# Performance work log

Hardware: AMD Instinct MI355X
Metric: run time of the kernel (lower is better)

Reference implementation:

```python
import jax, jax.numpy as jnp
import numpy as np

N_HEADS = 16
D_MODEL = 1024
D_K = D_MODEL // N_HEADS
B, S = 2, 2048


def setup_inputs() -> dict:
    key = jax.random.key(0)
    ks = jax.random.split(key, 12)
    sc = 1.0 / np.sqrt(D_MODEL)
    inp = {
        'query': jax.random.normal(ks[0], (B, S, D_MODEL), jnp.float32),
        'key':   jax.random.normal(ks[1], (B, S, D_MODEL), jnp.float32),
        'value': jax.random.normal(ks[2], (B, S, D_MODEL), jnp.float32),
        'mask':  jnp.ones((B, 1, 1, S), jnp.int32),
        'Wq': jax.random.normal(ks[3], (D_MODEL, D_MODEL), jnp.float32) * sc,
        'bq': jnp.zeros((D_MODEL,), jnp.float32),
        'Wk': jax.random.normal(ks[4], (D_MODEL, D_MODEL), jnp.float32) * sc,
        'bk': jnp.zeros((D_MODEL,), jnp.float32),
        'Wv': jax.random.normal(ks[5], (D_MODEL, D_MODEL), jnp.float32) * sc,
        'bv': jnp.zeros((D_MODEL,), jnp.float32),
        'Wo': jax.random.normal(ks[6], (D_MODEL, D_MODEL), jnp.float32) * sc,
        'bo': jnp.zeros((D_MODEL,), jnp.float32),
    }
    return inp


def reference(query, key, value, mask, Wq, bq, Wk, bk, Wv, bv, Wo, bo):
    # Linear projections (torch Linear: x @ W.T + b)
    q = query @ Wq.T + bq
    k = key @ Wk.T + bk
    v = value @ Wv.T + bv
    # [B, S, D] -> [B, H, S, d_k]
    def split_heads(x):
        b, s, _ = x.shape
        return x.reshape(b, s, N_HEADS, D_K).transpose(0, 2, 1, 3)
    q, k, v = split_heads(q), split_heads(k), split_heads(v)
    # scaled dot-product attention with explicit [B,H,S,S] scores
    att = jnp.einsum('bhqd,bhkd->bhqk', q, k) / jnp.sqrt(jnp.float32(D_K))
    att = jnp.where(mask == 0, -jnp.inf, att)
    scores = jax.nn.softmax(att, axis=-1)
    # dropout is identity in eval/reference mode
    out = jnp.einsum('bhqk,bhkd->bhqd', scores, v)
    b = out.shape[0]
    out = out.transpose(0, 2, 1, 3).reshape(b, -1, N_HEADS * D_K)
    return out @ Wo.T + bo
```

## Files before the change

kernel.cpp:

```cpp
#include <hip/hip_runtime.h>
#include <hip/hip_bf16.h>

#define DM   1024
#define SLEN 2048
#define NH   16
#define DK   64

typedef float f32x4 __attribute__((ext_vector_type(4)));
typedef short short8 __attribute__((ext_vector_type(8)));

__device__ __forceinline__ unsigned short f2bf(float f) {
  union { float f; unsigned int u; } x; x.f = f;
  unsigned int r = x.u + 0x7fffu + ((x.u >> 16) & 1u);
  return (unsigned short)(r >> 16);
}

__device__ __forceinline__ void gload_lds16(const unsigned short* g, unsigned short* l) {
  __builtin_amdgcn_global_load_lds(
      (const __attribute__((address_space(1))) unsigned int*)g,
      (__attribute__((address_space(3))) unsigned int*)l, 16, 0, 0);
}

struct ConvArgs { const float* src[7]; unsigned short* dst[7]; };

__global__ __launch_bounds__(256) void conv_kernel(ConvArgs a) {
  int blk = blockIdx.x, seg, base;
  if (blk < 6144) { seg = blk >> 11; base = blk & 2047; }
  else { int t = blk - 6144; seg = 3 + (t >> 9); base = t & 511; }
  const float* s = a.src[seg];
  unsigned short* d = a.dst[seg];
  int idx = (base * 256 + (int)threadIdx.x) * 8;
  float4 v0 = *(const float4*)(s + idx);
  float4 v1 = *(const float4*)(s + idx + 4);
  unsigned short o[8];
  o[0]=f2bf(v0.x); o[1]=f2bf(v0.y); o[2]=f2bf(v0.z); o[3]=f2bf(v0.w);
  o[4]=f2bf(v1.x); o[5]=f2bf(v1.y); o[6]=f2bf(v1.z); o[7]=f2bf(v1.w);
  *(uint4*)(d + idx) = *(uint4*)o;
}

template <int MODE>
__device__ __forceinline__ void gemm_core(const unsigned short* __restrict__ A,
                                          const unsigned short* __restrict__ W,
                                          const float* __restrict__ bias,
                                          void* __restrict__ outp, float scale,
                                          int m0, int n0,
                                          unsigned short* As, unsigned short* Bs) {
  const int tid = threadIdx.x;
  const int lane = tid & 63;
  const int wv = tid >> 6;
  const int wm = (wv >> 1) * 64, wn = (wv & 1) * 64;

  f32x4 acc[4][4];
#pragma unroll
  for (int i = 0; i < 4; ++i)
#pragma unroll
    for (int j = 0; j < 4; ++j) acc[i][j] = (f32x4){0.f, 0.f, 0.f, 0.f};

  for (int k0 = 0; k0 < DM; k0 += 32) {
    __syncthreads();
#pragma unroll
    for (int i = 0; i < 2; ++i) {
      int c = tid + i * 256;
      int row = c >> 2, cs = (c & 3) << 3;
      gload_lds16(A + (size_t)(m0 + row) * DM + k0 + cs, As + c * 8);
      gload_lds16(W + (size_t)(n0 + row) * DM + k0 + cs, Bs + c * 8);
    }
    __syncthreads();
    short8 af[4], bf[4];
#pragma unroll
    for (int i = 0; i < 4; ++i)
      af[i] = *(const short8*)(As + (wm + i * 16 + (lane & 15)) * 32 + ((lane >> 4) << 3));
#pragma unroll
    for (int j = 0; j < 4; ++j)
      bf[j] = *(const short8*)(Bs + (wn + j * 16 + (lane & 15)) * 32 + ((lane >> 4) << 3));
#pragma unroll
    for (int i = 0; i < 4; ++i)
#pragma unroll
      for (int j = 0; j < 4; ++j)
        acc[i][j] = __builtin_amdgcn_mfma_f32_16x16x32_bf16(af[i], bf[j], acc[i][j], 0, 0, 0);
  }

#pragma unroll
  for (int i = 0; i < 4; ++i)
#pragma unroll
    for (int j = 0; j < 4; ++j) {
      int col = n0 + wn + j * 16 + (lane & 15);
      float bv = bias[col];
      int row0 = m0 + wm + i * 16 + ((lane >> 4) << 2);
      if (MODE == 2) {
        unsigned short pk[4];
#pragma unroll
        for (int g = 0; g < 4; ++g) pk[g] = f2bf(acc[i][j][g] + bv);
        int d = col & (DK - 1), hh = col >> 6;
        int brow = row0 >> 11, srow = row0 & (SLEN - 1);
        size_t idx = ((size_t)((brow * NH + hh) * DK + d)) * SLEN + srow;
        *(uint2*)(((unsigned short*)outp) + idx) = *(uint2*)pk;
      } else {
#pragma unroll
        for (int g = 0; g < 4; ++g) {
          int row = row0 + g;
          float v = acc[i][j][g] + bv;
          if (MODE == 0) {
            v *= scale;
            size_t idx = ((size_t)((row >> 11) * NH + (col >> 6))) * (SLEN * DK) +
                         (size_t)(row & (SLEN - 1)) * DK + (col & (DK - 1));
            ((unsigned short*)outp)[idx] = f2bf(v);
          } else {
            ((float*)outp)[(size_t)row * DM + col] = v;
          }
        }
      }
    }
}

struct QKArgs {
  const unsigned short* A[2];
  const unsigned short* W[2];
  const float* bias[2];
  unsigned short* out[2];
  float scale[2];
};

__global__ __launch_bounds__(256) void gemm_qk_kernel(QKArgs a) {
  __shared__ unsigned short As[128 * 32], Bs[128 * 32];
  int z = blockIdx.z;
  gemm_core<0>(a.A[z], a.W[z], a.bias[z], a.out[z], a.scale[z],
               blockIdx.x * 128, blockIdx.y * 128, As, Bs);
}

__global__ __launch_bounds__(256) void gemm_v_kernel(const unsigned short* __restrict__ A,
                                                     const unsigned short* __restrict__ W,
                                                     const float* __restrict__ bias,
                                                     unsigned short* __restrict__ out) {
  __shared__ unsigned short As[128 * 32], Bs[128 * 32];
  gemm_core<2>(A, W, bias, out, 1.0f, blockIdx.x * 128, blockIdx.y * 128, As, Bs);
}

__global__ __launch_bounds__(256) void gemm_o_kernel(const unsigned short* __restrict__ A,
                                                     const unsigned short* __restrict__ W,
                                                     const float* __restrict__ bias,
                                                     float* __restrict__ out) {
  __shared__ unsigned short As[128 * 32], Bs[128 * 32];
  gemm_core<1>(A, W, bias, out, 1.0f, blockIdx.x * 128, blockIdx.y * 128, As, Bs);
}

__global__ __launch_bounds__(256) void attn_kernel(
    const unsigned short* __restrict__ Qw,
    const unsigned short* __restrict__ Kw,
    const unsigned short* __restrict__ Vtw,
    const int* __restrict__ mask,
    unsigned short* __restrict__ attn_out) {
  __shared__ unsigned short QPs[128 * 72];
  __shared__ unsigned short Ks[64 * 72];
  __shared__ unsigned short Vts[64 * 72];
  __shared__ float maskadd[64];

  const int tid = threadIdx.x;
  const int lane = tid & 63;
  const int wv = tid >> 6;
  const int s0 = blockIdx.x * 128;
  const int bh = blockIdx.y;
  const int b = bh >> 4, h = bh & 15;
  const unsigned short* Qb = Qw + (size_t)bh * (SLEN * DK);
  const unsigned short* Kb = Kw + (size_t)bh * (SLEN * DK);
  const unsigned short* Vtb = Vtw + (size_t)bh * (SLEN * DK);

#pragma unroll
  for (int i = 0; i < 4; ++i) {
    int seg = tid + i * 256;
    int row = seg >> 3, d0 = (seg & 7) << 3;
    *(uint4*)(QPs + row * 72 + d0) = *(const uint4*)(Qb + (size_t)(s0 + row) * DK + d0);
  }

  const int srow = tid >> 3, scol = (tid & 7) << 3;
  const int srow2 = (tid + 256) >> 3, scol2 = ((tid + 256) & 7) << 3;
  uint4 kreg[2], vreg[2];
  int mreg = 1;
  {
    kreg[0] = *(const uint4*)(Kb + (size_t)srow * DK + scol);
    kreg[1] = *(const uint4*)(Kb + (size_t)srow2 * DK + scol2);
    vreg[0] = *(const uint4*)(Vtb + (size_t)srow * SLEN + scol);
    vreg[1] = *(const uint4*)(Vtb + (size_t)srow2 * SLEN + scol2);
    if (tid < 64) mreg = mask[b * SLEN + tid];
  }

  __syncthreads();
  const int qb = wv * 32;
  short8 aq[2][2];
#pragma unroll
  for (int r = 0; r < 2; ++r)
#pragma unroll
    for (int ks = 0; ks < 2; ++ks)
      aq[r][ks] = *(const short8*)(QPs + (qb + r * 16 + (lane & 15)) * 72 + ks * 32 + ((lane >> 4) << 3));

  float lsum[2][4];
  f32x4 O[2][4];
#pragma unroll
  for (int r = 0; r < 2; ++r)
#pragma unroll
    for (int g = 0; g < 4; ++g) {
      lsum[r][g] = 0.f;
      O[r][g] = (f32x4){0.f, 0.f, 0.f, 0.f};
    }

  for (int kt = 0; kt < SLEN / 64; ++kt) {
    if (kt) __syncthreads();
    *(uint4*)(Ks + srow * 72 + scol) = kreg[0];
    *(uint4*)(Ks + srow2 * 72 + scol2) = kreg[1];
    *(uint4*)(Vts + srow * 72 + scol) = vreg[0];
    *(uint4*)(Vts + srow2 * 72 + scol2) = vreg[1];
    if (tid < 64) maskadd[tid] = mreg ? 0.0f : -1e30f;
    __syncthreads();
    if (kt < SLEN / 64 - 1) {
      const int kv1 = (kt + 1) * 64;
      kreg[0] = *(const uint4*)(Kb + (size_t)(kv1 + srow) * DK + scol);
      kreg[1] = *(const uint4*)(Kb + (size_t)(kv1 + srow2) * DK + scol2);
      vreg[0] = *(const uint4*)(Vtb + (size_t)srow * SLEN + kv1 + scol);
      vreg[1] = *(const uint4*)(Vtb + (size_t)srow2 * SLEN + kv1 + scol2);
      if (tid < 64) mreg = mask[b * SLEN + kv1 + tid];
    }

    f32x4 sc[2][4];
#pragma unroll
    for (int c = 0; c < 4; ++c) {
      short8 bk0 = *(const short8*)(Ks + (c * 16 + (lane & 15)) * 72 + ((lane >> 4) << 3));
      short8 bk1 = *(const short8*)(Ks + (c * 16 + (lane & 15)) * 72 + 32 + ((lane >> 4) << 3));
#pragma unroll
      for (int r = 0; r < 2; ++r) {
        f32x4 z = (f32x4){0.f, 0.f, 0.f, 0.f};
        z = __builtin_amdgcn_mfma_f32_16x16x32_bf16(aq[r][0], bk0, z, 0, 0, 0);
        sc[r][c] = __builtin_amdgcn_mfma_f32_16x16x32_bf16(aq[r][1], bk1, z, 0, 0, 0);
      }
    }

    __hip_bfloat16* Pp = (__hip_bfloat16*)QPs;
#pragma unroll
    for (int c = 0; c < 4; ++c) {
      float ma = maskadd[c * 16 + (lane & 15)];
      int colp = c * 16 + (lane & 15);
#pragma unroll
      for (int r = 0; r < 2; ++r) {
        float p0 = __builtin_exp2f(sc[r][c][0] + ma);
        float p1 = __builtin_exp2f(sc[r][c][1] + ma);
        float p2 = __builtin_exp2f(sc[r][c][2] + ma);
        float p3 = __builtin_exp2f(sc[r][c][3] + ma);
        lsum[r][0] += p0; lsum[r][1] += p1; lsum[r][2] += p2; lsum[r][3] += p3;
        __hip_bfloat162 h01 = __float22bfloat162_rn(float2{p0, p1});
        __hip_bfloat162 h23 = __float22bfloat162_rn(float2{p2, p3});
        int row0 = qb + r * 16 + ((lane >> 4) << 2);
        Pp[(row0 + 0) * 72 + colp] = h01.x;
        Pp[(row0 + 1) * 72 + colp] = h01.y;
        Pp[(row0 + 2) * 72 + colp] = h23.x;
        Pp[(row0 + 3) * 72 + colp] = h23.y;
      }
    }

    short8 ap[2][2];
#pragma unroll
    for (int r = 0; r < 2; ++r)
#pragma unroll
      for (int ks = 0; ks < 2; ++ks)
        ap[r][ks] = *(const short8*)(QPs + (qb + r * 16 + (lane & 15)) * 72 + ks * 32 + ((lane >> 4) << 3));
#pragma unroll
    for (int dt = 0; dt < 4; ++dt) {
      short8 bv0 = *(const short8*)(Vts + (dt * 16 + (lane & 15)) * 72 + ((lane >> 4) << 3));
      short8 bv1 = *(const short8*)(Vts + (dt * 16 + (lane & 15)) * 72 + 32 + ((lane >> 4) << 3));
#pragma unroll
      for (int r = 0; r < 2; ++r) {
        O[r][dt] = __builtin_amdgcn_mfma_f32_16x16x32_bf16(ap[r][0], bv0, O[r][dt], 0, 0, 0);
        O[r][dt] = __builtin_amdgcn_mfma_f32_16x16x32_bf16(ap[r][1], bv1, O[r][dt], 0, 0, 0);
      }
    }
  }

#pragma unroll
  for (int r = 0; r < 2; ++r)
#pragma unroll
    for (int g = 0; g < 4; ++g) {
      float rs = lsum[r][g];
      rs += __shfl_xor(rs, 1);
      rs += __shfl_xor(rs, 2);
      rs += __shfl_xor(rs, 4);
      rs += __shfl_xor(rs, 8);
      float inv = 1.0f / rs;
      int row = s0 + qb + r * 16 + ((lane >> 4) << 2) + g;
#pragma unroll
      for (int dt = 0; dt < 4; ++dt) {
        int col = h * DK + dt * 16 + (lane & 15);
        attn_out[(size_t)(b * SLEN + row) * DM + col] = f2bf(O[r][dt][g] * inv);
      }
    }
}

extern "C" void kernel_launch(void* const* d_in, const int* in_sizes, int n_in,
                              void* d_out, int out_size, void* d_ws, size_t ws_size,
                              hipStream_t stream) {
  (void)in_sizes; (void)n_in; (void)out_size; (void)ws_size;
  const float* query = (const float*)d_in[0];
  const float* key_  = (const float*)d_in[1];
  const float* value = (const float*)d_in[2];
  const int*   mask  = (const int*)d_in[3];
  const float* Wq = (const float*)d_in[4];
  const float* bq = (const float*)d_in[5];
  const float* Wk = (const float*)d_in[6];
  const float* bk = (const float*)d_in[7];
  const float* Wv = (const float*)d_in[8];
  const float* bv = (const float*)d_in[9];
  const float* Wo = (const float*)d_in[10];
  const float* bo = (const float*)d_in[11];
  float* out = (float*)d_out;

  const size_t WSZ = 1048576, XSZ = 4194304;
  unsigned short* base = (unsigned short*)d_ws;
  unsigned short* Wqb = base;
  unsigned short* Wkb = base + WSZ;
  unsigned short* Wvb = base + 2 * WSZ;
  unsigned short* Wob = base + 3 * WSZ;
  unsigned short* Xqb = base + 4 * WSZ;
  unsigned short* Xkb = Xqb + XSZ;
  unsigned short* Xvb = Xqb + 2 * XSZ;
  unsigned short* Qw  = Xqb + 3 * XSZ;
  unsigned short* Kw  = Qw + XSZ;
  unsigned short* Vtw = Qw + 2 * XSZ;
  unsigned short* attnb = Qw + 3 * XSZ;

  ConvArgs ca;
  ca.src[0] = query; ca.src[1] = key_; ca.src[2] = value;
  ca.src[3] = Wq; ca.src[4] = Wk; ca.src[5] = Wv; ca.src[6] = Wo;
  ca.dst[0] = Xqb; ca.dst[1] = Xkb; ca.dst[2] = Xvb;
  ca.dst[3] = Wqb; ca.dst[4] = Wkb; ca.dst[5] = Wvb; ca.dst[6] = Wob;
  conv_kernel<<<8192, 256, 0, stream>>>(ca);

  QKArgs qa;
  qa.A[0] = Xqb; qa.A[1] = Xkb;
  qa.W[0] = Wqb; qa.W[1] = Wkb;
  qa.bias[0] = bq; qa.bias[1] = bk;
  qa.out[0] = Qw; qa.out[1] = Kw;
  qa.scale[0] = 0.18033688011112042f;
  qa.scale[1] = 1.0f;
  gemm_qk_kernel<<<dim3(32, 8, 2), 256, 0, stream>>>(qa);
  gemm_v_kernel<<<dim3(32, 8), 256, 0, stream>>>(Xvb, Wvb, bv, Vtw);

  attn_kernel<<<dim3(16, 32), 256, 0, stream>>>(Qw, Kw, Vtw, mask, attnb);

  gemm_o_kernel<<<dim3(32, 8), 256, 0, stream>>>(attnb, Wob, bo, out);
}
```

Baseline: 295.6 us.

## Merge QKV GEMM launches, halve O-GEMM tile N, use 8 waves in attention

The V projection now runs in the same launch as Q and K, selected by a runtime mode per z-slice, which removes one launch and lets the three projections share the GPU. The output projection uses 128x64 tiles, doubling its block count for better CU fill. The attention kernel runs 512 threads with each wave owning 16 query rows instead of 32. This halves per-wave register state and raises the wave count, but each K/V tile is now reused by fewer MFMAs per wave.

```diff
diff --git a/kernel.cpp b/kernel.cpp
--- a/kernel.cpp
+++ b/kernel.cpp
@@ -38,8 +38,9 @@
   *(uint4*)(d + idx) = *(uint4*)o;
 }
 
-template <int MODE>
-__device__ __forceinline__ void gemm_core(const unsigned short* __restrict__ A,
+template <int TN>
+__device__ __forceinline__ void gemm_core(int mode,
+                                          const unsigned short* __restrict__ A,
                                           const unsigned short* __restrict__ W,
                                           const float* __restrict__ bias,
                                           void* __restrict__ outp, float scale,
@@ -48,46 +49,50 @@
   const int tid = threadIdx.x;
   const int lane = tid & 63;
   const int wv = tid >> 6;
-  const int wm = (wv >> 1) * 64, wn = (wv & 1) * 64;
-
-  f32x4 acc[4][4];
+  const int wm = (wv >> 1) * 64, wn = (wv & 1) * (TN / 2);
+  const int NB = TN / 32;
+
+  f32x4 acc[4][NB];
 #pragma unroll
   for (int i = 0; i < 4; ++i)
 #pragma unroll
-    for (int j = 0; j < 4; ++j) acc[i][j] = (f32x4){0.f, 0.f, 0.f, 0.f};
+    for (int j = 0; j < NB; ++j) acc[i][j] = (f32x4){0.f, 0.f, 0.f, 0.f};
 
   for (int k0 = 0; k0 < DM; k0 += 32) {
     __syncthreads();
 #pragma unroll
     for (int i = 0; i < 2; ++i) {
       int c = tid + i * 256;
-      int row = c >> 2, cs = (c & 3) << 3;
-      gload_lds16(A + (size_t)(m0 + row) * DM + k0 + cs, As + c * 8);
-      gload_lds16(W + (size_t)(n0 + row) * DM + k0 + cs, Bs + c * 8);
+      gload_lds16(A + (size_t)(m0 + (c >> 2)) * DM + k0 + ((c & 3) << 3), As + c * 8);
+    }
+#pragma unroll
+    for (int i = 0; i < TN / 64; ++i) {
+      int c = tid + i * 256;
+      gload_lds16(W + (size_t)(n0 + (c >> 2)) * DM + k0 + ((c & 3) << 3), Bs + c * 8);
     }
     __syncthreads();
-    short8 af[4], bf[4];
+    short8 af[4], bf[NB];
 #pragma unroll
     for (int i = 0; i < 4; ++i)
       af[i] = *(const short8*)(As + (wm + i * 16 + (lane & 15)) * 32 + ((lane >> 4) << 3));
 #pragma unroll
-    for (int j = 0; j < 4; ++j)
+    for (int j = 0; j < NB; ++j)
       bf[j] = *(const short8*)(Bs + (wn + j * 16 + (lane & 15)) * 32 + ((lane >> 4) << 3));
 #pragma unroll
     for (int i = 0; i < 4; ++i)
 #pragma unroll
-      for (int j = 0; j < 4; ++j)
+      for (int j = 0; j < NB; ++j)
         acc[i][j] = __builtin_amdgcn_mfma_f32_16x16x32_bf16(af[i], bf[j], acc[i][j], 0, 0, 0);
   }
 
 #pragma unroll
   for (int i = 0; i < 4; ++i)
 #pragma unroll
-    for (int j = 0; j < 4; ++j) {
+    for (int j = 0; j < NB; ++j) {
       int col = n0 + wn + j * 16 + (lane & 15);
       float bv = bias[col];
-      int row0 = m0 + wm + i * 16 + ((lane >> 4) << 2);
-      if (MODE == 2) {
+      int row0 = wm + i * 16 + ((lane >> 4) << 2) + m0;
+      if (mode == 2) {
         unsigned short pk[4];
 #pragma unroll
         for (int g = 0; g < 4; ++g) pk[g] = f2bf(acc[i][j][g] + bv);
@@ -95,56 +100,48 @@
         int brow = row0 >> 11, srow = row0 & (SLEN - 1);
         size_t idx = ((size_t)((brow * NH + hh) * DK + d)) * SLEN + srow;
         *(uint2*)(((unsigned short*)outp) + idx) = *(uint2*)pk;
-      } else {
+      } else if (mode == 0) {
 #pragma unroll
         for (int g = 0; g < 4; ++g) {
           int row = row0 + g;
-          float v = acc[i][j][g] + bv;
-          if (MODE == 0) {
-            v *= scale;
-            size_t idx = ((size_t)((row >> 11) * NH + (col >> 6))) * (SLEN * DK) +
-                         (size_t)(row & (SLEN - 1)) * DK + (col & (DK - 1));
-            ((unsigned short*)outp)[idx] = f2bf(v);
-          } else {
-            ((float*)outp)[(size_t)row * DM + col] = v;
-          }
+          float v = (acc[i][j][g] + bv) * scale;
+          size_t idx = ((size_t)((row >> 11) * NH + (col >> 6))) * (SLEN * DK) +
+                       (size_t)(row & (SLEN - 1)) * DK + (col & (DK - 1));
+          ((unsigned short*)outp)[idx] = f2bf(v);
         }
+      } else {
+#pragma unroll
+        for (int g = 0; g < 4; ++g)
+          ((float*)outp)[(size_t)(row0 + g) * DM + col] = acc[i][j][g] + bv;
       }
     }
 }
 
-struct QKArgs {
-  const unsigned short* A[2];
-  const unsigned short* W[2];
-  const float* bias[2];
-  unsigned short* out[2];
-  float scale[2];
+struct QKVArgs {
+  const unsigned short* A[3];
+  const unsigned short* W[3];
+  const float* bias[3];
+  unsigned short* out[3];
+  float scale[3];
+  int mode[3];
 };
 
-__global__ __launch_bounds__(256) void gemm_qk_kernel(QKArgs a) {
+__global__ __launch_bounds__(256) void gemm_qkv_kernel(QKVArgs a) {
   __shared__ unsigned short As[128 * 32], Bs[128 * 32];
   int z = blockIdx.z;
-  gemm_core<0>(a.A[z], a.W[z], a.bias[z], a.out[z], a.scale[z],
-               blockIdx.x * 128, blockIdx.y * 128, As, Bs);
-}
-
-__global__ __launch_bounds__(256) void gemm_v_kernel(const unsigned short* __restrict__ A,
-                                                     const unsigned short* __restrict__ W,
-                                                     const float* __restrict__ bias,
-                                                     unsigned short* __restrict__ out) {
-  __shared__ unsigned short As[128 * 32], Bs[128 * 32];
-  gemm_core<2>(A, W, bias, out, 1.0f, blockIdx.x * 128, blockIdx.y * 128, As, Bs);
+  gemm_core<128>(a.mode[z], a.A[z], a.W[z], a.bias[z], a.out[z], a.scale[z],
+                 blockIdx.x * 128, blockIdx.y * 128, As, Bs);
 }
 
 __global__ __launch_bounds__(256) void gemm_o_kernel(const unsigned short* __restrict__ A,
                                                      const unsigned short* __restrict__ W,
                                                      const float* __restrict__ bias,
                                                      float* __restrict__ out) {
-  __shared__ unsigned short As[128 * 32], Bs[128 * 32];
-  gemm_core<1>(A, W, bias, out, 1.0f, blockIdx.x * 128, blockIdx.y * 128, As, Bs);
-}
-
-__global__ __launch_bounds__(256) void attn_kernel(
+  __shared__ unsigned short As[128 * 32], Bs[64 * 32];
+  gemm_core<64>(1, A, W, bias, out, 1.0f, blockIdx.x * 128, blockIdx.y * 64, As, Bs);
+}
+
+__global__ __launch_bounds__(512) void attn_kernel(
     const unsigned short* __restrict__ Qw,
     const unsigned short* __restrict__ Kw,
     const unsigned short* __restrict__ Vtw,
@@ -166,130 +163,99 @@
   const unsigned short* Vtb = Vtw + (size_t)bh * (SLEN * DK);
 
 #pragma unroll
-  for (int i = 0; i < 4; ++i) {
-    int seg = tid + i * 256;
+  for (int i = 0; i < 2; ++i) {
+    int seg = tid + i * 512;
     int row = seg >> 3, d0 = (seg & 7) << 3;
     *(uint4*)(QPs + row * 72 + d0) = *(const uint4*)(Qb + (size_t)(s0 + row) * DK + d0);
   }
 
   const int srow = tid >> 3, scol = (tid & 7) << 3;
-  const int srow2 = (tid + 256) >> 3, scol2 = ((tid + 256) & 7) << 3;
-  uint4 kreg[2], vreg[2];
-  int mreg = 1;
-  {
-    kreg[0] = *(const uint4*)(Kb + (size_t)srow * DK + scol);
-    kreg[1] = *(const uint4*)(Kb + (size_t)srow2 * DK + scol2);
-    vreg[0] = *(const uint4*)(Vtb + (size_t)srow * SLEN + scol);
-    vreg[1] = *(const uint4*)(Vtb + (size_t)srow2 * SLEN + scol2);
-    if (tid < 64) mreg = mask[b * SLEN + tid];
-  }
+  uint4 kreg = *(const uint4*)(Kb + (size_t)srow * DK + scol);
+  uint4 vreg = *(const uint4*)(Vtb + (size_t)srow * SLEN + scol);
+  int mreg = (tid < 64) ? mask[b * SLEN + tid] : 1;
 
   __syncthreads();
-  const int qb = wv * 32;
-  short8 aq[2][2];
-#pragma unroll
-  for (int r = 0; r < 2; ++r)
-#pragma unroll
-    for (int ks = 0; ks < 2; ++ks)
-      aq[r][ks] = *(const short8*)(QPs + (qb + r * 16 + (lane & 15)) * 72 + ks * 32 + ((lane >> 4) << 3));
-
-  float lsum[2][4];
-  f32x4 O[2][4];
-#pragma unroll
-  for (int r = 0; r < 2; ++r)
-#pragma unroll
-    for (int g = 0; g < 4; ++g) {
-      lsum[r][g] = 0.f;
-      O[r][g] = (f32x4){0.f, 0.f, 0.f, 0.f};
-    }
+  const int qb = wv * 16;
+  short8 aq[2];
+#pragma unroll
+  for (int ks = 0; ks < 2; ++ks)
+    aq[ks] = *(const short8*)(QPs + (qb + (lane & 15)) * 72 + ks * 32 + ((lane >> 4) << 3));
+
+  float lsum[4] = {0.f, 0.f, 0.f, 0.f};
+  f32x4 O[4];
+#pragma unroll
+  for (int dt = 0; dt < 4; ++dt) O[dt] = (f32x4){0.f, 0.f, 0.f, 0.f};
 
   for (int kt = 0; kt < SLEN / 64; ++kt) {
     if (kt) __syncthreads();
-    *(uint4*)(Ks + srow * 72 + scol) = kreg[0];
-    *(uint4*)(Ks + srow2 * 72 + scol2) = kreg[1];
-    *(uint4*)(Vts + srow * 72 + scol) = vreg[0];
-    *(uint4*)(Vts + srow2 * 72 + scol2) = vreg[1];
+    *(uint4*)(Ks + srow * 72 + scol) = kreg;
+    *(uint4*)(Vts + srow * 72 + scol) = vreg;
     if (tid < 64) maskadd[tid] = mreg ? 0.0f : -1e30f;
     __syncthreads();
     if (kt < SLEN / 64 - 1) {
       const int kv1 = (kt + 1) * 64;
-      kreg[0] = *(const uint4*)(Kb + (size_t)(kv1 + srow) * DK + scol);
-      kreg[1] = *(const uint4*)(Kb + (size_t)(kv1 + srow2) * DK + scol2);
-      vreg[0] = *(const uint4*)(Vtb + (size_t)srow * SLEN + kv1 + scol);
-      vreg[1] = *(const uint4*)(Vtb + (size_t)srow2 * SLEN + kv1 + scol2);
+      kreg = *(const uint4*)(Kb + (size_t)(kv1 + srow) * DK + scol);
+      vreg = *(const uint4*)(Vtb + (size_t)srow * SLEN + kv1 + scol);
       if (tid < 64) mreg = mask[b * SLEN + kv1 + tid];
     }
 
-    f32x4 sc[2][4];
+    f32x4 sc[4];
 #pragma unroll
     for (int c = 0; c < 4; ++c) {
       short8 bk0 = *(const short8*)(Ks + (c * 16 + (lane & 15)) * 72 + ((lane >> 4) << 3));
       short8 bk1 = *(const short8*)(Ks + (c * 16 + (lane & 15)) * 72 + 32 + ((lane >> 4) << 3));
-#pragma unroll
-      for (int r = 0; r < 2; ++r) {
-        f32x4 z = (f32x4){0.f, 0.f, 0.f, 0.f};
-        z = __builtin_amdgcn_mfma_f32_16x16x32_bf16(aq[r][0], bk0, z, 0, 0, 0);
-        sc[r][c] = __builtin_amdgcn_mfma_f32_16x16x32_bf16(aq[r][1], bk1, z, 0, 0, 0);
-      }
+      f32x4 z = (f32x4){0.f, 0.f, 0.f, 0.f};
+      z = __builtin_amdgcn_mfma_f32_16x16x32_bf16(aq[0], bk0, z, 0, 0, 0);
+      sc[c] = __builtin_amdgcn_mfma_f32_16x16x32_bf16(aq[1], bk1, z, 0, 0, 0);
     }
 
     __hip_bfloat16* Pp = (__hip_bfloat16*)QPs;
+    const int row0 = qb + ((lane >> 4) << 2);
 #pragma unroll
     for (int c = 0; c < 4; ++c) {
-      float ma = maskadd[c * 16 + (lane & 15)];
       int colp = c * 16 + (lane & 15);
-#pragma unroll
-      for (int r = 0; r < 2; ++r) {
-        float p0 = __builtin_exp2f(sc[r][c][0] + ma);
-        float p1 = __builtin_exp2f(sc[r][c][1] + ma);
-        float p2 = __builtin_exp2f(sc[r][c][2] + ma);
-        float p3 = __builtin_exp2f(sc[r][c][3] + ma);
-        lsum[r][0] += p0; lsum[r][1] += p1; lsum[r][2] += p2; lsum[r][3] += p3;
-        __hip_bfloat162 h01 = __float22bfloat162_rn(float2{p0, p1});
-        __hip_bfloat162 h23 = __float22bfloat162_rn(float2{p2, p3});
-        int row0 = qb + r * 16 + ((lane >> 4) << 2);
-        Pp[(row0 + 0) * 72 + colp] = h01.x;
-        Pp[(row0 + 1) * 72 + colp] = h01.y;
-        Pp[(row0 + 2) * 72 + colp] = h23.x;
-        Pp[(row0 + 3) * 72 + colp] = h23.y;
-      }
-    }
-
-    short8 ap[2][2];
-#pragma unroll
-    for (int r = 0; r < 2; ++r)
-#pragma unroll
-      for (int ks = 0; ks < 2; ++ks)
-        ap[r][ks] = *(const short8*)(QPs + (qb + r * 16 + (lane & 15)) * 72 + ks * 32 + ((lane >> 4) << 3));
+      float ma = maskadd[colp];
+      float p0 = __builtin_exp2f(sc[c][0] + ma);
+      float p1 = __builtin_exp2f(sc[c][1] + ma);
+      float p2 = __builtin_exp2f(sc[c][2] + ma);
+      float p3 = __builtin_exp2f(sc[c][3] + ma);
+      lsum[0] += p0; lsum[1] += p1; lsum[2] += p2; lsum[3] += p3;
+      __hip_bfloat162 h01 = __float22bfloat162_rn(float2{p0, p1});
+      __hip_bfloat162 h23 = __float22bfloat162_rn(float2{p2, p3});
+      Pp[(row0 + 0) * 72 + colp] = h01.x;
+      Pp[(row0 + 1) * 72 + colp] = h01.y;
+      Pp[(row0 + 2) * 72 + colp] = h23.x;
+      Pp[(row0 + 3) * 72 + colp] = h23.y;
+    }
+
+    short8 ap[2];
+#pragma unroll
+    for (int ks = 0; ks < 2; ++ks)
+      ap[ks] = *(const short8*)(QPs + (qb + (lane & 15)) * 72 + ks * 32 + ((lane >> 4) << 3));
 #pragma unroll
     for (int dt = 0; dt < 4; ++dt) {
       short8 bv0 = *(const short8*)(Vts + (dt * 16 + (lane & 15)) * 72 + ((lane >> 4) << 3));
       short8 bv1 = *(const short8*)(Vts + (dt * 16 + (lane & 15)) * 72 + 32 + ((lane >> 4) << 3));
-#pragma unroll
-      for (int r = 0; r < 2; ++r) {
-        O[r][dt] = __builtin_amdgcn_mfma_f32_16x16x32_bf16(ap[r][0], bv0, O[r][dt], 0, 0, 0);
-        O[r][dt] = __builtin_amdgcn_mfma_f32_16x16x32_bf16(ap[r][1], bv1, O[r][dt], 0, 0, 0);
-      }
+      O[dt] = __builtin_amdgcn_mfma_f32_16x16x32_bf16(ap[0], bv0, O[dt], 0, 0, 0);
+      O[dt] = __builtin_amdgcn_mfma_f32_16x16x32_bf16(ap[1], bv1, O[dt], 0, 0, 0);
     }
   }
 
 #pragma unroll
-  for (int r = 0; r < 2; ++r)
-#pragma unroll
-    for (int g = 0; g < 4; ++g) {
-      float rs = lsum[r][g];
-      rs += __shfl_xor(rs, 1);
-      rs += __shfl_xor(rs, 2);
-      rs += __shfl_xor(rs, 4);
-      rs += __shfl_xor(rs, 8);
-      float inv = 1.0f / rs;
-      int row = s0 + qb + r * 16 + ((lane >> 4) << 2) + g;
-#pragma unroll
-      for (int dt = 0; dt < 4; ++dt) {
-        int col = h * DK + dt * 16 + (lane & 15);
-        attn_out[(size_t)(b * SLEN + row) * DM + col] = f2bf(O[r][dt][g] * inv);
-      }
-    }
+  for (int g = 0; g < 4; ++g) {
+    float rs = lsum[g];
+    rs += __shfl_xor(rs, 1);
+    rs += __shfl_xor(rs, 2);
+    rs += __shfl_xor(rs, 4);
+    rs += __shfl_xor(rs, 8);
+    float inv = 1.0f / rs;
+    int row = s0 + qb + ((lane >> 4) << 2) + g;
+#pragma unroll
+    for (int dt = 0; dt < 4; ++dt) {
+      int col = h * DK + dt * 16 + (lane & 15);
+      attn_out[(size_t)(b * SLEN + row) * DM + col] = f2bf(O[dt][g] * inv);
+    }
+  }
 }
 
 extern "C" void kernel_launch(void* const* d_in, const int* in_sizes, int n_in,
@@ -331,17 +297,17 @@
   ca.dst[3] = Wqb; ca.dst[4] = Wkb; ca.dst[5] = Wvb; ca.dst[6] = Wob;
   conv_kernel<<<8192, 256, 0, stream>>>(ca);
 
-  QKArgs qa;
-  qa.A[0] = Xqb; qa.A[1] = Xkb;
-  qa.W[0] = Wqb; qa.W[1] = Wkb;
-  qa.bias[0] = bq; qa.bias[1] = bk;
-  qa.out[0] = Qw; qa.out[1] = Kw;
+  QKVArgs qa;
+  qa.A[0] = Xqb; qa.A[1] = Xkb; qa.A[2] = Xvb;
+  qa.W[0] = Wqb; qa.W[1] = Wkb; qa.W[2] = Wvb;
+  qa.bias[0] = bq; qa.bias[1] = bk; qa.bias[2] = bv;
+  qa.out[0] = Qw; qa.out[1] = Kw; qa.out[2] = Vtw;
   qa.scale[0] = 0.18033688011112042f;
-  qa.scale[1] = 1.0f;
-  gemm_qk_kernel<<<dim3(32, 8, 2), 256, 0, stream>>>(qa);
-  gemm_v_kernel<<<dim3(32, 8), 256, 0, stream>>>(Xvb, Wvb, bv, Vtw);
-
-  attn_kernel<<<dim3(16, 32), 256, 0, stream>>>(Qw, Kw, Vtw, mask, attnb);
-
-  gemm_o_kernel<<<dim3(32, 8), 256, 0, stream>>>(attnb, Wob, bo, out);
-}
+  qa.scale[1] = 1.0f; qa.scale[2] = 1.0f;
+  qa.mode[0] = 0; qa.mode[1] = 0; qa.mode[2] = 2;
+  gemm_qkv_kernel<<<dim3(32, 8, 3), 256, 0, stream>>>(qa);
+
+  attn_kernel<<<dim3(16, 32), 512, 0, stream>>>(Qw, Kw, Vtw, mask, attnb);
+
+  gemm_o_kernel<<<dim3(32, 16), 256, 0, stream>>>(attnb, Wob, bo, out);
+}
```

Measured after the change: 256.6 us. 13.2% less time.
